# Kernel optimization log

Hardware: AMD Instinct MI355X
Metric: run time of the kernel (lower is better)

The kernel has to match this reference:

```python
import jax, jax.numpy as jnp
import numpy as np

T = 1_000_000
DT = 1e-3  # uniform t_eval spacing; integration horizon t in [0, 1000)


def setup_inputs() -> dict:
    return {
        "t_eval": jnp.arange(T, dtype=jnp.float32) * DT,
        "x0": jnp.array([0.15, 0.08, 0.05], dtype=jnp.float32),
        "log_eps": jnp.float32(-2.0),
        "log_delta": jnp.float32(-0.5),
        "theta": jnp.full((3,), 0.1, dtype=jnp.float32),
        "readout_w": jnp.eye(3, dtype=jnp.float32),   # nn.init.eye_
        "readout_b": jnp.zeros((3,), dtype=jnp.float32),
    }


def _build_W(log_eps, log_delta, dtype):
    # W[i,j] = 0 if i==j; -1+eps if i==(j+1)%3; else -1-delta
    eps = jnp.exp(log_eps)
    delta = jnp.exp(log_delta)
    eye = jnp.eye(3, dtype=dtype)
    cyc = jnp.array([[0, 0, 1], [1, 0, 0], [0, 1, 0]], dtype=dtype)  # i == (j+1)%3
    return cyc * (-1.0 + eps) + (1.0 - eye - cyc) * (-1.0 - delta)


def _integrate(t_eval, x0, log_eps, log_delta, theta):
    """Dormand-Prince 5(4) stages, one fixed step per t_eval interval (dopri5 tableau)."""
    W = _build_W(log_eps, log_delta, x0.dtype)

    def f(x):  # autonomous CTLN RHS: -x + relu(W x + theta)
        return -x + jax.nn.relu(W @ x + theta)

    def step(x, dt):
        k1 = f(x)
        k2 = f(x + dt * (1.0 / 5.0 * k1))
        k3 = f(x + dt * (3.0 / 40.0 * k1 + 9.0 / 40.0 * k2))
        k4 = f(x + dt * (44.0 / 45.0 * k1 - 56.0 / 15.0 * k2 + 32.0 / 9.0 * k3))
        k5 = f(x + dt * (19372.0 / 6561.0 * k1 - 25360.0 / 2187.0 * k2
                         + 64448.0 / 6561.0 * k3 - 212.0 / 729.0 * k4))
        k6 = f(x + dt * (9017.0 / 3168.0 * k1 - 355.0 / 33.0 * k2
                         + 46732.0 / 5247.0 * k3 + 49.0 / 176.0 * k4
                         - 5103.0 / 18656.0 * k5))
        x_new = x + dt * (35.0 / 384.0 * k1 + 500.0 / 1113.0 * k3
                          + 125.0 / 192.0 * k4 - 2187.0 / 6784.0 * k5
                          + 11.0 / 84.0 * k6)
        return x_new, x_new

    dts = jnp.diff(t_eval)                       # [T-1]
    _, xs = jax.lax.scan(step, x0, dts)          # [T-1, 3]
    return jnp.concatenate([x0[None, :], xs], axis=0)  # [T, 3]


def reference(t_eval, x0, log_eps, log_delta, theta, readout_w, readout_b):
    traj = _integrate(t_eval, x0, log_eps, log_delta, theta)  # [T, 3]
    pred = traj @ readout_w.T + readout_b                      # Linear(3,3)
    return traj, pred
```

## Files before the change

### kernel.cpp

```cpp
#include <hip/hip_runtime.h>
#include <hip/hip_cooperative_groups.h>
#include <math.h>

namespace cg = cooperative_groups;


#define C21 (1.0/5.0)
#define C31 (3.0/40.0)
#define C32 (9.0/40.0)
#define C41 (44.0/45.0)
#define C42 (-56.0/15.0)
#define C43 (32.0/9.0)
#define C51 (19372.0/6561.0)
#define C52 (-25360.0/2187.0)
#define C53 (64448.0/6561.0)
#define C54 (-212.0/729.0)
#define C61 (9017.0/3168.0)
#define C62 (-355.0/33.0)
#define C63 (46732.0/5247.0)
#define C64 (49.0/176.0)
#define C65 (-5103.0/18656.0)
#define B1  (35.0/384.0)
#define B3  (500.0/1113.0)
#define B4  (125.0/192.0)
#define B5  (-2187.0/6784.0)
#define B6  (11.0/84.0)

#define FT 256
#define FT_LOG2 8
#define FCH 16
#define NITER 4

struct MapF { float A[9]; float b[3]; };

__device__ inline void map_identity(MapF& m) {
#pragma unroll
  for (int i = 0; i < 9; ++i) m.A[i] = 0.f;
  m.A[0] = m.A[4] = m.A[8] = 1.f;
  m.b[0] = m.b[1] = m.b[2] = 0.f;
}

__device__ inline void map_compose(MapF& out, const MapF& m2, const MapF& m1) {
#pragma unroll
  for (int r = 0; r < 3; ++r) {
#pragma unroll
    for (int c = 0; c < 3; ++c)
      out.A[r*3+c] = m2.A[r*3+0]*m1.A[0+c] + m2.A[r*3+1]*m1.A[3+c] + m2.A[r*3+2]*m1.A[6+c];
    out.b[r] = m2.A[r*3+0]*m1.b[0] + m2.A[r*3+1]*m1.b[1] + m2.A[r*3+2]*m1.b[2] + m2.b[r];
  }
}

__device__ inline void map_apply(const MapF& m, const float x[3], float y[3]) {
#pragma unroll
  for (int r = 0; r < 3; ++r)
    y[r] = m.A[r*3+0]*x[0] + m.A[r*3+1]*x[1] + m.A[r*3+2]*x[2] + m.b[r];
}

__device__ inline MapF map_shfl_up(const MapF& m, int off) {
  MapF r;
#pragma unroll
  for (int i = 0; i < 9; ++i) r.A[i] = __shfl_up(m.A[i], off, 64);
#pragma unroll
  for (int i = 0; i < 3; ++i) r.b[i] = __shfl_up(m.b[i], off, 64);
  return r;
}

template <typename T, bool RECORD>
__device__ inline void stage_k(const T z[3], const T th[3],
                               T wa, T wb, T g[3], T k[3]) {
  T y0 = fma(wa, z[2], fma(wb, z[1], th[0]));
  T y1 = fma(wa, z[0], fma(wb, z[2], th[1]));
  T y2 = fma(wa, z[1], fma(wb, z[0], th[2]));
  if (RECORD) {
    g[0] = (y0 > T(0)) ? T(1) : T(0);
    g[1] = (y1 > T(0)) ? T(1) : T(0);
    g[2] = (y2 > T(0)) ? T(1) : T(0);
  }
  k[0] = y0 * g[0] - z[0];
  k[1] = y1 * g[1] - z[1];
  k[2] = y2 * g[2] - z[2];
}

template <typename T, bool RECORD>
__device__ inline void dopri_eval(const T v[3], const T th[3], T dt,
                                  T wa, T wb, T G[6][3], T out[3]) {
  T k1[3], k2[3], k3[3], k4[3], k5[3], k6[3], z[3];
  stage_k<T, RECORD>(v, th, wa, wb, G[0], k1);
  const T d21 = dt * T(C21);
#pragma unroll
  for (int c = 0; c < 3; ++c) z[c] = fma(d21, k1[c], v[c]);
  stage_k<T, RECORD>(z, th, wa, wb, G[1], k2);
#pragma unroll
  for (int c = 0; c < 3; ++c) z[c] = fma(dt, fma(T(C31), k1[c], T(C32) * k2[c]), v[c]);
  stage_k<T, RECORD>(z, th, wa, wb, G[2], k3);
#pragma unroll
  for (int c = 0; c < 3; ++c)
    z[c] = fma(dt, fma(T(C41), k1[c], fma(T(C42), k2[c], T(C43) * k3[c])), v[c]);
  stage_k<T, RECORD>(z, th, wa, wb, G[3], k4);
#pragma unroll
  for (int c = 0; c < 3; ++c)
    z[c] = fma(dt, fma(T(C51), k1[c], fma(T(C52), k2[c], fma(T(C53), k3[c], T(C54) * k4[c]))), v[c]);
  stage_k<T, RECORD>(z, th, wa, wb, G[4], k5);
#pragma unroll
  for (int c = 0; c < 3; ++c)
    z[c] = fma(dt, fma(T(C61), k1[c], fma(T(C62), k2[c], fma(T(C63), k3[c], fma(T(C64), k4[c], T(C65) * k5[c])))), v[c]);
  stage_k<T, RECORD>(z, th, wa, wb, G[5], k6);
#pragma unroll
  for (int c = 0; c < 3; ++c)
    out[c] = fma(dt, fma(T(B1), k1[c], fma(T(B3), k3[c], fma(T(B4), k4[c], fma(T(B5), k5[c], T(B6) * k6[c])))), v[c]);
}

__device__ inline void build_map_step(float x[3], float dt, float wa, float wb,
                                      const float th[3], MapF& m) {
  float G[6][3], xn[3];
  dopri_eval<float, true>(x, th, dt, wa, wb, G, xn);
  const float z3[3] = {0.f, 0.f, 0.f};
  dopri_eval<float, false>(z3, th, dt, wa, wb, G, m.b);
  float e[3], col[3];
#pragma unroll
  for (int j = 0; j < 3; ++j) {
    e[0] = 0.f; e[1] = 0.f; e[2] = 0.f; e[j] = 1.f;
    dopri_eval<float, false>(e, z3, dt, wa, wb, G, col);
    m.A[0 + j] = col[0];
    m.A[3 + j] = col[1];
    m.A[6 + j] = col[2];
  }
  x[0] = xn[0]; x[1] = xn[1]; x[2] = xn[2];
}

__device__ inline void block_scan(MapF run, MapF& P, MapF& tot,
                                  MapF* wtot, int lane, int wid) {
#pragma unroll
  for (int off = 1; off < 64; off <<= 1) {
    MapF nb = map_shfl_up(run, off);
    MapF c; map_compose(c, run, nb);
    if (lane >= off) run = c;
  }
  __syncthreads();
  if (lane == 63) wtot[wid] = run;
  __syncthreads();
  MapF wpre; map_identity(wpre);
  for (int w = 0; w < wid; ++w) { MapF t2; map_compose(t2, wtot[w], wpre); wpre = t2; }
  MapF excl = map_shfl_up(run, 1);
  if (lane == 0) map_identity(excl);
  map_compose(P, excl, wpre);
  map_compose(tot, run, wpre);
}

__device__ inline void group_walk(float xs[3], const float dtg[FCH],
                                  float wa, float wb, const float th[3],
                                  MapF& run) {
  map_identity(run);
  MapF mp, tmp;
  float x[3] = {xs[0], xs[1], xs[2]};
#pragma unroll
  for (int s = 0; s < FCH; ++s) {
    build_map_step(x, dtg[s], wa, wb, th, mp);
    map_compose(tmp, mp, run);
    run = tmp;
  }
}

__device__ inline void load_dtg(const float* __restrict__ t_eval, int n0, int T,
                                float dtg[FCH], float& tv0) {
  int i0 = n0 > T - 1 ? T - 1 : n0;
  tv0 = t_eval[i0];
  float prev = tv0;
#pragma unroll
  for (int s = 1; s <= FCH; ++s) {
    int idx = n0 + s; if (idx > T - 1) idx = T - 1;
    float c = t_eval[idx];
    dtg[s - 1] = c - prev;
    prev = c;
  }
}


__global__ void k_coarse(const float* __restrict__ x0f,
                         const float* __restrict__ le, const float* __restrict__ ld,
                         const float* __restrict__ thf,
                         float* __restrict__ cst, int NC, float dtc) {
  if (threadIdx.x != 0 || blockIdx.x != 0) return;
  const float a = -1.f + expf(le[0]);
  const float b = -1.f - expf(ld[0]);
  const float t0 = thf[0], t1 = thf[1], t2 = thf[2];
  float x = x0f[0], y = x0f[1], z = x0f[2];
  cst[0] = x; cst[1] = y; cst[2] = z;
  const float dt = dtc, dth = 0.5f * dtc, dt6 = dtc * (1.f / 6.f);
#define RHSF(px, py, pz, kx, ky, kz)                      \
  do {                                                    \
    float y0_ = fmaf(a, (pz), fmaf(b, (py), t0));         \
    float y1_ = fmaf(a, (px), fmaf(b, (pz), t1));         \
    float y2_ = fmaf(a, (py), fmaf(b, (px), t2));         \
    (kx) = fmaxf(y0_, 0.f) - (px);                        \
    (ky) = fmaxf(y1_, 0.f) - (py);                        \
    (kz) = fmaxf(y2_, 0.f) - (pz);                        \
  } while (0)
  for (int i = 1; i <= NC; ++i) {
    float k1x,k1y,k1z,k2x,k2y,k2z,k3x,k3y,k3z,k4x,k4y,k4z,zx,zy,zz;
    RHSF(x, y, z, k1x, k1y, k1z);
    zx = fmaf(dth, k1x, x); zy = fmaf(dth, k1y, y); zz = fmaf(dth, k1z, z);
    RHSF(zx, zy, zz, k2x, k2y, k2z);
    zx = fmaf(dth, k2x, x); zy = fmaf(dth, k2y, y); zz = fmaf(dth, k2z, z);
    RHSF(zx, zy, zz, k3x, k3y, k3z);
    zx = fmaf(dt, k3x, x); zy = fmaf(dt, k3y, y); zz = fmaf(dt, k3z, z);
    RHSF(zx, zy, zz, k4x, k4y, k4z);
    x = fmaf(dt6, k1x + 2.f*k2x + 2.f*k3x + k4x, x);
    y = fmaf(dt6, k1y + 2.f*k2y + 2.f*k3y + k4y, y);
    z = fmaf(dt6, k1z + 2.f*k2z + 2.f*k3z + k4z, z);
    cst[3*i] = x; cst[3*i+1] = y; cst[3*i+2] = z;
  }
#undef RHSF
}

__global__ __launch_bounds__(FT) void k_mega(
    const float* __restrict__ t_eval, const float* __restrict__ seedst,
    const float* __restrict__ x0f,
    const float* __restrict__ le, const float* __restrict__ ld,
    const float* __restrict__ thf,
    float* __restrict__ gstart,
    MapF* __restrict__ btot, MapF* __restrict__ bpre,
    int S, int T, int NG1, int NB, float hseed, int nstates) {
  cg::grid_group grid = cg::this_grid();
  __shared__ MapF wtot[FT / 64];

  const int t = threadIdx.x;
  const int lane = t & 63, wid = t >> 6;
  const int g = blockIdx.x * FT + t;
  const bool active = (g < NG1);
  const int n0 = g * FCH;

  const float wa = -1.f + expf(le[0]);
  const float wb = -1.f - expf(ld[0]);
  const float th[3] = {thf[0], thf[1], thf[2]};
  const float x0d[3] = {x0f[0], x0f[1], x0f[2]};

  float dtg[FCH];
  float xs[3] = {0.f, 0.f, 0.f};
  if (active) {
    float tv0;
    load_dtg(t_eval, n0, T, dtg, tv0);
    float u = tv0 / hseed;
    int j = (int)u;
    if (j < 0) j = 0;
    if (j > nstates - 2) j = nstates - 2;
    float f = u - (float)j;
#pragma unroll
    for (int c = 0; c < 3; ++c) {
      float a0 = seedst[3*j + c], b0 = seedst[3*(j+1) + c];
      xs[c] = a0 + f * (b0 - a0);
    }
  } else {
#pragma unroll
    for (int s = 0; s < FCH; ++s) dtg[s] = 0.f;
  }
  if (g == 0) { xs[0] = x0d[0]; xs[1] = x0d[1]; xs[2] = x0d[2]; }

  for (int it = 0; it < NITER; ++it) {
    MapF run;
    if (active) group_walk(xs, dtg, wa, wb, th, run);
    else map_identity(run);

    MapF P, tot;
    block_scan(run, P, tot, wtot, lane, wid);
    if (t == FT - 1) btot[blockIdx.x] = tot;
    grid.sync();

    if (blockIdx.x == 0) {
      MapF rb;
      if (t < NB) rb = btot[t]; else map_identity(rb);
      MapF Pb, totb;
      block_scan(rb, Pb, totb, wtot, lane, wid);
      if (t < NB) bpre[t] = Pb;
    }
    grid.sync();

    {
      MapF bp = bpre[blockIdx.x];
      MapF Pn; map_compose(Pn, P, bp);
      float ns[3]; map_apply(Pn, x0d, ns);
      if (active && g != 0) { xs[0] = ns[0]; xs[1] = ns[1]; xs[2] = ns[2]; }
    }
  }

  if (active) {
    gstart[3*g]   = xs[0];
    gstart[3*g+1] = xs[1];
    gstart[3*g+2] = xs[2];
  }
}

__global__ __launch_bounds__(256) void k_polish(
    const float* __restrict__ t_eval, const float* __restrict__ gstart,
    const float* __restrict__ x0f,
    const float* __restrict__ le, const float* __restrict__ ld,
    const float* __restrict__ thf,
    const float* __restrict__ row, const float* __restrict__ rob,
    float* __restrict__ traj, float* __restrict__ pred, int S, int T, int NG1) {
  const int g = blockIdx.x * blockDim.x + threadIdx.x;
  if (g >= NG1) return;
  const int n0 = g * FCH;
  float dtg[FCH]; float tv0;
  load_dtg(t_eval, n0, T, dtg, tv0);

  const double wa = -1.0 + exp((double)le[0]);
  const double wb = -1.0 - exp((double)ld[0]);
  const double th[3] = {(double)thf[0], (double)thf[1], (double)thf[2]};
  const float w00 = row[0], w01 = row[1], w02 = row[2];
  const float w10 = row[3], w11 = row[4], w12 = row[5];
  const float w20 = row[6], w21 = row[7], w22 = row[8];
  const float b0 = rob[0], b1 = rob[1], b2 = rob[2];

  double x[3];
  if (g == 0) {
    x[0] = (double)x0f[0]; x[1] = (double)x0f[1]; x[2] = (double)x0f[2];
    float a0 = x0f[0], a1 = x0f[1], a2 = x0f[2];
    traj[0] = a0; traj[1] = a1; traj[2] = a2;
    pred[0] = fmaf(w00, a0, fmaf(w01, a1, fmaf(w02, a2, b0)));
    pred[1] = fmaf(w10, a0, fmaf(w11, a1, fmaf(w12, a2, b1)));
    pred[2] = fmaf(w20, a0, fmaf(w21, a1, fmaf(w22, a2, b2)));
  } else {
    x[0] = (double)gstart[3*g]; x[1] = (double)gstart[3*g+1]; x[2] = (double)gstart[3*g+2];
  }

  double G[6][3], xn[3];
#pragma unroll
  for (int s = 0; s < FCH; ++s) {
    dopri_eval<double, true>(x, th, (double)dtg[s], wa, wb, G, xn);
    x[0] = xn[0]; x[1] = xn[1]; x[2] = xn[2];
    int n = n0 + s;
    if (n < S) {
      float a0 = (float)x[0], a1 = (float)x[1], a2 = (float)x[2];
      traj[3*(n+1)]   = a0;
      traj[3*(n+1)+1] = a1;
      traj[3*(n+1)+2] = a2;
      pred[3*(n+1)]   = fmaf(w00, a0, fmaf(w01, a1, fmaf(w02, a2, b0)));
      pred[3*(n+1)+1] = fmaf(w10, a0, fmaf(w11, a1, fmaf(w12, a2, b1)));
      pred[3*(n+1)+2] = fmaf(w20, a0, fmaf(w21, a1, fmaf(w22, a2, b2)));
    }
  }
}


__global__ void k_start0(const float* __restrict__ t_eval,
                         const float* __restrict__ seedst,
                         const float* __restrict__ x0f,
                         float* __restrict__ gs, int T, int NG1,
                         float hseed, int nstates) {
  int g = blockIdx.x * blockDim.x + threadIdx.x;
  if (g >= NG1) return;
  if (g == 0) { gs[0] = x0f[0]; gs[1] = x0f[1]; gs[2] = x0f[2]; return; }
  int n0 = g * FCH; if (n0 > T - 1) n0 = T - 1;
  float u = t_eval[n0] / hseed;
  int j = (int)u;
  if (j < 0) j = 0;
  if (j > nstates - 2) j = nstates - 2;
  float f = u - (float)j;
#pragma unroll
  for (int c = 0; c < 3; ++c) {
    float a0 = seedst[3*j + c], b0 = seedst[3*(j+1) + c];
    gs[3*g + c] = a0 + f * (b0 - a0);
  }
}

__global__ __launch_bounds__(FT) void k_up_fb(
    const float* __restrict__ t_eval, const float* __restrict__ gs,
    const float* __restrict__ le, const float* __restrict__ ld,
    const float* __restrict__ thf,
    MapF* __restrict__ lpre, MapF* __restrict__ btot, int T, int NG1) {
  __shared__ MapF wtot[FT / 64];
  const int t = threadIdx.x, lane = t & 63, wid = t >> 6;
  const int g = blockIdx.x * FT + t;
  const bool active = (g < NG1);
  const float wa = -1.f + expf(le[0]);
  const float wb = -1.f - expf(ld[0]);
  const float th[3] = {thf[0], thf[1], thf[2]};
  MapF run;
  if (active) {
    float dtg[FCH]; float tv0;
    load_dtg(t_eval, g * FCH, T, dtg, tv0);
    float xs[3] = {gs[3*g], gs[3*g+1], gs[3*g+2]};
    group_walk(xs, dtg, wa, wb, th, run);
  } else map_identity(run);
  MapF P, tot;
  block_scan(run, P, tot, wtot, lane, wid);
  if (active) lpre[g] = P;
  if (t == FT - 1) btot[blockIdx.x] = tot;
}

__global__ __launch_bounds__(FT) void k_bscan_fb(const MapF* __restrict__ btot,
                                                 MapF* __restrict__ bpre, int NB) {
  __shared__ MapF wtot[FT / 64];
  const int t = threadIdx.x, lane = t & 63, wid = t >> 6;
  MapF run;
  if (t < NB) run = btot[t]; else map_identity(run);
  MapF P, tot;
  block_scan(run, P, tot, wtot, lane, wid);
  if (t < NB) bpre[t] = P;
}

__global__ void k_fold_fb(const MapF* __restrict__ lpre, const MapF* __restrict__ bpre,
                          const float* __restrict__ x0f,
                          float* __restrict__ gsout, int NG1) {
  int g = blockIdx.x * blockDim.x + threadIdx.x;
  if (g >= NG1) return;
  if (g == 0) { gsout[0] = x0f[0]; gsout[1] = x0f[1]; gsout[2] = x0f[2]; return; }
  MapF P;
  map_compose(P, lpre[g], bpre[g >> FT_LOG2]);
  float x0d[3] = {x0f[0], x0f[1], x0f[2]}, ns[3];
  map_apply(P, x0d, ns);
  gsout[3*g] = ns[0]; gsout[3*g+1] = ns[1]; gsout[3*g+2] = ns[2];
}


extern "C" void kernel_launch(void* const* d_in, const int* in_sizes, int n_in,
                              void* d_out, int out_size, void* d_ws, size_t ws_size,
                              hipStream_t stream) {
  const float* t_eval    = (const float*)d_in[0];
  const float* x0        = (const float*)d_in[1];
  const float* log_eps   = (const float*)d_in[2];
  const float* log_delta = (const float*)d_in[3];
  const float* theta     = (const float*)d_in[4];
  const float* readout_w = (const float*)d_in[5];
  const float* readout_b = (const float*)d_in[6];

  int T_   = in_sizes[0];
  int S_   = T_ - 1;
  int NG1_ = (S_ + FCH - 1) / FCH;
  int NB_  = (NG1_ + FT - 1) / FT;

  const float DTS_SEED = 0.45f;
  const int   NSEED    = (int)(((double)S_ * 1e-3) / (double)DTS_SEED) + 2;
  int nstates_ = NSEED + 1;
  float hseed_ = DTS_SEED;

  float* trajh = (float*)d_out;
  float* predh = trajh + (size_t)3 * T_;

  char* w = (char*)d_ws;
  float* seedst = (float*)w;  w += (((size_t)3 * (NSEED + 1) * 4) + 255) & ~(size_t)255;
  float* gsA    = (float*)w;  w += (((size_t)3 * NG1_ * 4) + 255) & ~(size_t)255;
  float* gsB    = (float*)w;  w += (((size_t)3 * NG1_ * 4) + 255) & ~(size_t)255;
  MapF* lpre    = (MapF*)w;   w += (((size_t)NG1_ * sizeof(MapF)) + 255) & ~(size_t)255;
  MapF* btot    = (MapF*)w;   w += (((size_t)NB_ * sizeof(MapF)) + 255) & ~(size_t)255;
  MapF* bpre    = (MapF*)w;

  k_coarse<<<1, 64, 0, stream>>>(x0, log_eps, log_delta, theta, seedst, NSEED, DTS_SEED);

  const float* t_eval_ = t_eval;
  const float* seedst_ = seedst;
  const float* x0_ = x0;
  const float* le_ = log_eps;
  const float* ld_ = log_delta;
  const float* th_ = theta;
  float* gs_ = gsA;
  MapF* btot_ = btot;
  MapF* bpre_ = bpre;

  void* args[] = {
    (void*)&t_eval_, (void*)&seedst_, (void*)&x0_, (void*)&le_, (void*)&ld_,
    (void*)&th_, (void*)&gs_, (void*)&btot_, (void*)&bpre_,
    (void*)&S_, (void*)&T_, (void*)&NG1_, (void*)&NB_,
    (void*)&hseed_, (void*)&nstates_,
  };
  hipError_t cerr = hipLaunchCooperativeKernel((const void*)k_mega, dim3(NB_), dim3(FT),
                                               args, 0, stream);
  const float* finalgs = gsA;
  if (cerr != hipSuccess) {
    k_start0<<<(NG1_ + 255) / 256, 256, 0, stream>>>(t_eval, seedst, x0, gsA,
                                                     T_, NG1_, hseed_, nstates_);
    float* cur = gsA; float* nxt = gsB;
    for (int it = 0; it < NITER; ++it) {
      k_up_fb<<<NB_, FT, 0, stream>>>(t_eval, cur, log_eps, log_delta, theta,
                                      lpre, btot, T_, NG1_);
      k_bscan_fb<<<1, FT, 0, stream>>>(btot, bpre, NB_);
      k_fold_fb<<<(NG1_ + 255) / 256, 256, 0, stream>>>(lpre, bpre, x0, nxt, NG1_);
      float* tmp = cur; cur = nxt; nxt = tmp;
    }
    finalgs = cur;
  }

  k_polish<<<(NG1_ + 255) / 256, 256, 0, stream>>>(t_eval, finalgs, x0,
                                                   log_eps, log_delta, theta,
                                                   readout_w, readout_b,
                                                   trajh, predh, S_, T_, NG1_);
}
```

Before: 740.5 us.

## Replace cooperative grid-sync mega kernel with decoupled look-back scan per iteration

Drops the cooperative kernel that used two grid-wide syncs per Newton iteration. Each iteration is now a separate launch that does its block-level map scan and then a single-pass decoupled look-back across blocks using flag, aggregate and inclusive buffers. The chunk size per thread is halved, which doubles the number of groups and blocks, and the coarse seed step is enlarged. This removes grid barriers and the block-0 serial scan, but adds kernel launches and a look-back spin that assumes earlier blocks make forward progress. One __syncthreads in block_scan is also removed, which could race on the shared wtot buffer across calls.

```diff
diff --git a/kernel.cpp b/kernel.cpp
--- a/kernel.cpp
+++ b/kernel.cpp
@@ -1,8 +1,5 @@
 #include <hip/hip_runtime.h>
-#include <hip/hip_cooperative_groups.h>
 #include <math.h>
-
-namespace cg = cooperative_groups;
 
 
 #define C21 (1.0/5.0)
@@ -27,8 +24,7 @@
 #define B6  (11.0/84.0)
 
 #define FT 256
-#define FT_LOG2 8
-#define FCH 16
+#define FCH 8
 #define NITER 4
 
 struct MapF { float A[9]; float b[3]; };
@@ -136,7 +132,6 @@
     MapF c; map_compose(c, run, nb);
     if (lane >= off) run = c;
   }
-  __syncthreads();
   if (lane == 63) wtot[wid] = run;
   __syncthreads();
   MapF wpre; map_identity(wpre);
@@ -145,20 +140,6 @@
   if (lane == 0) map_identity(excl);
   map_compose(P, excl, wpre);
   map_compose(tot, run, wpre);
-}
-
-__device__ inline void group_walk(float xs[3], const float dtg[FCH],
-                                  float wa, float wb, const float th[3],
-                                  MapF& run) {
-  map_identity(run);
-  MapF mp, tmp;
-  float x[3] = {xs[0], xs[1], xs[2]};
-#pragma unroll
-  for (int s = 0; s < FCH; ++s) {
-    build_map_step(x, dtg[s], wa, wb, th, mp);
-    map_compose(tmp, mp, run);
-    run = tmp;
-  }
 }
 
 __device__ inline void load_dtg(const float* __restrict__ t_eval, int n0, int T,
@@ -213,80 +194,119 @@
 #undef RHSF
 }
 
-__global__ __launch_bounds__(FT) void k_mega(
-    const float* __restrict__ t_eval, const float* __restrict__ seedst,
+__global__ void k_start0(const float* __restrict__ t_eval,
+                         const float* __restrict__ seedst,
+                         const float* __restrict__ x0f,
+                         float* __restrict__ gs, int* __restrict__ flags,
+                         int nflags, int T, int NG1, float hseed, int nstates) {
+  int g = blockIdx.x * blockDim.x + threadIdx.x;
+  if (g < nflags) flags[g] = 0;
+  if (g >= NG1) return;
+  if (g == 0) { gs[0] = x0f[0]; gs[1] = x0f[1]; gs[2] = x0f[2]; return; }
+  int n0 = g * FCH; if (n0 > T - 1) n0 = T - 1;
+  float u = t_eval[n0] / hseed;
+  int j = (int)u;
+  if (j < 0) j = 0;
+  if (j > nstates - 2) j = nstates - 2;
+  float f = u - (float)j;
+#pragma unroll
+  for (int c = 0; c < 3; ++c) {
+    float a0 = seedst[3*j + c], b0 = seedst[3*(j+1) + c];
+    gs[3*g + c] = a0 + f * (b0 - a0);
+  }
+}
+
+__global__ __launch_bounds__(FT) void k_iter(
+    const float* __restrict__ t_eval,
+    const float* __restrict__ gs_in, float* __restrict__ gs_out,
     const float* __restrict__ x0f,
     const float* __restrict__ le, const float* __restrict__ ld,
     const float* __restrict__ thf,
-    float* __restrict__ gstart,
-    MapF* __restrict__ btot, MapF* __restrict__ bpre,
-    int S, int T, int NG1, int NB, float hseed, int nstates) {
-  cg::grid_group grid = cg::this_grid();
+    MapF* __restrict__ aggp, MapF* __restrict__ inclp, int* __restrict__ flags,
+    int T, int NG1, int NB) {
   __shared__ MapF wtot[FT / 64];
-
-  const int t = threadIdx.x;
-  const int lane = t & 63, wid = t >> 6;
-  const int g = blockIdx.x * FT + t;
+  __shared__ MapF sAgg;
+  __shared__ MapF sE;
+
+  const int t = threadIdx.x, lane = t & 63, wid = t >> 6;
+  const int bid = blockIdx.x;
+  const int g = bid * FT + t;
   const bool active = (g < NG1);
-  const int n0 = g * FCH;
 
   const float wa = -1.f + expf(le[0]);
   const float wb = -1.f - expf(ld[0]);
   const float th[3] = {thf[0], thf[1], thf[2]};
   const float x0d[3] = {x0f[0], x0f[1], x0f[2]};
 
-  float dtg[FCH];
-  float xs[3] = {0.f, 0.f, 0.f};
+  MapF run;
   if (active) {
-    float tv0;
-    load_dtg(t_eval, n0, T, dtg, tv0);
-    float u = tv0 / hseed;
-    int j = (int)u;
-    if (j < 0) j = 0;
-    if (j > nstates - 2) j = nstates - 2;
-    float f = u - (float)j;
-#pragma unroll
-    for (int c = 0; c < 3; ++c) {
-      float a0 = seedst[3*j + c], b0 = seedst[3*(j+1) + c];
-      xs[c] = a0 + f * (b0 - a0);
+    float dtg[FCH]; float tv0;
+    load_dtg(t_eval, g * FCH, T, dtg, tv0);
+    float x[3] = {gs_in[3*g], gs_in[3*g+1], gs_in[3*g+2]};
+    map_identity(run);
+    MapF mp, tmp;
+#pragma unroll
+    for (int s = 0; s < FCH; ++s) {
+      build_map_step(x, dtg[s], wa, wb, th, mp);
+      map_compose(tmp, mp, run);
+      run = tmp;
     }
   } else {
-#pragma unroll
-    for (int s = 0; s < FCH; ++s) dtg[s] = 0.f;
-  }
-  if (g == 0) { xs[0] = x0d[0]; xs[1] = x0d[1]; xs[2] = x0d[2]; }
-
-  for (int it = 0; it < NITER; ++it) {
-    MapF run;
-    if (active) group_walk(xs, dtg, wa, wb, th, run);
-    else map_identity(run);
-
-    MapF P, tot;
-    block_scan(run, P, tot, wtot, lane, wid);
-    if (t == FT - 1) btot[blockIdx.x] = tot;
-    grid.sync();
-
-    if (blockIdx.x == 0) {
-      MapF rb;
-      if (t < NB) rb = btot[t]; else map_identity(rb);
-      MapF Pb, totb;
-      block_scan(rb, Pb, totb, wtot, lane, wid);
-      if (t < NB) bpre[t] = Pb;
+    map_identity(run);
+  }
+
+  MapF P, tot;
+  block_scan(run, P, tot, wtot, lane, wid);
+
+  if (t == FT - 1) {
+    sAgg = tot;
+    aggp[bid] = tot;
+    __hip_atomic_store(&flags[bid], 1, __ATOMIC_RELEASE, __HIP_MEMORY_SCOPE_AGENT);
+  }
+  __syncthreads();
+
+  if (t == 0) {
+    MapF E;
+    if (bid == 0) {
+      map_identity(E);
+    } else {
+      MapF A; map_identity(A);
+      int j = bid - 1;
+      while (true) {
+        int f;
+        do {
+          f = __hip_atomic_load(&flags[j], __ATOMIC_ACQUIRE, __HIP_MEMORY_SCOPE_AGENT);
+          if (f == 0) __builtin_amdgcn_s_sleep(1);
+        } while (f == 0);
+        if (f == 2) {
+          MapF inc = inclp[j];
+          MapF E2; map_compose(E2, A, inc);
+          E = E2;
+          break;
+        } else {
+          MapF ag = aggp[j];
+          MapF A2; map_compose(A2, A, ag);
+          A = A2;
+          --j;
+          if (j < 0) { E = A; break; }
+        }
+      }
     }
-    grid.sync();
-
-    {
-      MapF bp = bpre[blockIdx.x];
-      MapF Pn; map_compose(Pn, P, bp);
-      float ns[3]; map_apply(Pn, x0d, ns);
-      if (active && g != 0) { xs[0] = ns[0]; xs[1] = ns[1]; xs[2] = ns[2]; }
-    }
-  }
+    sE = E;
+    MapF inc; map_compose(inc, sAgg, E);
+    inclp[bid] = inc;
+    __hip_atomic_store(&flags[bid], 2, __ATOMIC_RELEASE, __HIP_MEMORY_SCOPE_AGENT);
+  }
+  __syncthreads();
 
   if (active) {
-    gstart[3*g]   = xs[0];
-    gstart[3*g+1] = xs[1];
-    gstart[3*g+2] = xs[2];
+    MapF E = sE;
+    MapF Pg; map_compose(Pg, P, E);
+    float ns[3]; map_apply(Pg, x0d, ns);
+    if (g == 0) { ns[0] = x0d[0]; ns[1] = x0d[1]; ns[2] = x0d[2]; }
+    gs_out[3*g]   = ns[0];
+    gs_out[3*g+1] = ns[1];
+    gs_out[3*g+2] = ns[2];
   }
 }
 
@@ -342,77 +362,6 @@
 }
 
 
-__global__ void k_start0(const float* __restrict__ t_eval,
-                         const float* __restrict__ seedst,
-                         const float* __restrict__ x0f,
-                         float* __restrict__ gs, int T, int NG1,
-                         float hseed, int nstates) {
-  int g = blockIdx.x * blockDim.x + threadIdx.x;
-  if (g >= NG1) return;
-  if (g == 0) { gs[0] = x0f[0]; gs[1] = x0f[1]; gs[2] = x0f[2]; return; }
-  int n0 = g * FCH; if (n0 > T - 1) n0 = T - 1;
-  float u = t_eval[n0] / hseed;
-  int j = (int)u;
-  if (j < 0) j = 0;
-  if (j > nstates - 2) j = nstates - 2;
-  float f = u - (float)j;
-#pragma unroll
-  for (int c = 0; c < 3; ++c) {
-    float a0 = seedst[3*j + c], b0 = seedst[3*(j+1) + c];
-    gs[3*g + c] = a0 + f * (b0 - a0);
-  }
-}
-
-__global__ __launch_bounds__(FT) void k_up_fb(
-    const float* __restrict__ t_eval, const float* __restrict__ gs,
-    const float* __restrict__ le, const float* __restrict__ ld,
-    const float* __restrict__ thf,
-    MapF* __restrict__ lpre, MapF* __restrict__ btot, int T, int NG1) {
-  __shared__ MapF wtot[FT / 64];
-  const int t = threadIdx.x, lane = t & 63, wid = t >> 6;
-  const int g = blockIdx.x * FT + t;
-  const bool active = (g < NG1);
-  const float wa = -1.f + expf(le[0]);
-  const float wb = -1.f - expf(ld[0]);
-  const float th[3] = {thf[0], thf[1], thf[2]};
-  MapF run;
-  if (active) {
-    float dtg[FCH]; float tv0;
-    load_dtg(t_eval, g * FCH, T, dtg, tv0);
-    float xs[3] = {gs[3*g], gs[3*g+1], gs[3*g+2]};
-    group_walk(xs, dtg, wa, wb, th, run);
-  } else map_identity(run);
-  MapF P, tot;
-  block_scan(run, P, tot, wtot, lane, wid);
-  if (active) lpre[g] = P;
-  if (t == FT - 1) btot[blockIdx.x] = tot;
-}
-
-__global__ __launch_bounds__(FT) void k_bscan_fb(const MapF* __restrict__ btot,
-                                                 MapF* __restrict__ bpre, int NB) {
-  __shared__ MapF wtot[FT / 64];
-  const int t = threadIdx.x, lane = t & 63, wid = t >> 6;
-  MapF run;
-  if (t < NB) run = btot[t]; else map_identity(run);
-  MapF P, tot;
-  block_scan(run, P, tot, wtot, lane, wid);
-  if (t < NB) bpre[t] = P;
-}
-
-__global__ void k_fold_fb(const MapF* __restrict__ lpre, const MapF* __restrict__ bpre,
-                          const float* __restrict__ x0f,
-                          float* __restrict__ gsout, int NG1) {
-  int g = blockIdx.x * blockDim.x + threadIdx.x;
-  if (g >= NG1) return;
-  if (g == 0) { gsout[0] = x0f[0]; gsout[1] = x0f[1]; gsout[2] = x0f[2]; return; }
-  MapF P;
-  map_compose(P, lpre[g], bpre[g >> FT_LOG2]);
-  float x0d[3] = {x0f[0], x0f[1], x0f[2]}, ns[3];
-  map_apply(P, x0d, ns);
-  gsout[3*g] = ns[0]; gsout[3*g+1] = ns[1]; gsout[3*g+2] = ns[2];
-}
-
-
 extern "C" void kernel_launch(void* const* d_in, const int* in_sizes, int n_in,
                               void* d_out, int out_size, void* d_ws, size_t ws_size,
                               hipStream_t stream) {
@@ -429,7 +378,7 @@
   int NG1_ = (S_ + FCH - 1) / FCH;
   int NB_  = (NG1_ + FT - 1) / FT;
 
-  const float DTS_SEED = 0.45f;
+  const float DTS_SEED = 0.6f;
   const int   NSEED    = (int)(((double)S_ * 1e-3) / (double)DTS_SEED) + 2;
   int nstates_ = NSEED + 1;
   float hseed_ = DTS_SEED;
@@ -441,46 +390,26 @@
   float* seedst = (float*)w;  w += (((size_t)3 * (NSEED + 1) * 4) + 255) & ~(size_t)255;
   float* gsA    = (float*)w;  w += (((size_t)3 * NG1_ * 4) + 255) & ~(size_t)255;
   float* gsB    = (float*)w;  w += (((size_t)3 * NG1_ * 4) + 255) & ~(size_t)255;
-  MapF* lpre    = (MapF*)w;   w += (((size_t)NG1_ * sizeof(MapF)) + 255) & ~(size_t)255;
-  MapF* btot    = (MapF*)w;   w += (((size_t)NB_ * sizeof(MapF)) + 255) & ~(size_t)255;
-  MapF* bpre    = (MapF*)w;
+  MapF* aggp    = (MapF*)w;   w += (((size_t)NITER * NB_ * sizeof(MapF)) + 255) & ~(size_t)255;
+  MapF* inclp   = (MapF*)w;   w += (((size_t)NITER * NB_ * sizeof(MapF)) + 255) & ~(size_t)255;
+  int* flags    = (int*)w;    w += (((size_t)NITER * NB_ * 4) + 255) & ~(size_t)255;
+  const int nflags = NITER * NB_;
 
   k_coarse<<<1, 64, 0, stream>>>(x0, log_eps, log_delta, theta, seedst, NSEED, DTS_SEED);
-
-  const float* t_eval_ = t_eval;
-  const float* seedst_ = seedst;
-  const float* x0_ = x0;
-  const float* le_ = log_eps;
-  const float* ld_ = log_delta;
-  const float* th_ = theta;
-  float* gs_ = gsA;
-  MapF* btot_ = btot;
-  MapF* bpre_ = bpre;
-
-  void* args[] = {
-    (void*)&t_eval_, (void*)&seedst_, (void*)&x0_, (void*)&le_, (void*)&ld_,
-    (void*)&th_, (void*)&gs_, (void*)&btot_, (void*)&bpre_,
-    (void*)&S_, (void*)&T_, (void*)&NG1_, (void*)&NB_,
-    (void*)&hseed_, (void*)&nstates_,
-  };
-  hipError_t cerr = hipLaunchCooperativeKernel((const void*)k_mega, dim3(NB_), dim3(FT),
-                                               args, 0, stream);
-  const float* finalgs = gsA;
-  if (cerr != hipSuccess) {
-    k_start0<<<(NG1_ + 255) / 256, 256, 0, stream>>>(t_eval, seedst, x0, gsA,
-                                                     T_, NG1_, hseed_, nstates_);
-    float* cur = gsA; float* nxt = gsB;
-    for (int it = 0; it < NITER; ++it) {
-      k_up_fb<<<NB_, FT, 0, stream>>>(t_eval, cur, log_eps, log_delta, theta,
-                                      lpre, btot, T_, NG1_);
-      k_bscan_fb<<<1, FT, 0, stream>>>(btot, bpre, NB_);
-      k_fold_fb<<<(NG1_ + 255) / 256, 256, 0, stream>>>(lpre, bpre, x0, nxt, NG1_);
-      float* tmp = cur; cur = nxt; nxt = tmp;
-    }
-    finalgs = cur;
-  }
-
-  k_polish<<<(NG1_ + 255) / 256, 256, 0, stream>>>(t_eval, finalgs, x0,
+  k_start0<<<(NG1_ + 255) / 256, 256, 0, stream>>>(t_eval, seedst, x0, gsA, flags,
+                                                   nflags, T_, NG1_, hseed_, nstates_);
+
+  float* cur = gsA; float* nxt = gsB;
+  for (int it = 0; it < NITER; ++it) {
+    k_iter<<<NB_, FT, 0, stream>>>(t_eval, cur, nxt, x0, log_eps, log_delta, theta,
+                                   aggp + (size_t)it * NB_,
+                                   inclp + (size_t)it * NB_,
+                                   flags + (size_t)it * NB_,
+                                   T_, NG1_, NB_);
+    float* tmp = cur; cur = nxt; nxt = tmp;
+  }
+
+  k_polish<<<(NG1_ + 255) / 256, 256, 0, stream>>>(t_eval, cur, x0,
                                                    log_eps, log_delta, theta,
                                                    readout_w, readout_b,
                                                    trajh, predh, S_, T_, NG1_);
```

Result: slower. 768.4 us (+3.8%).
